# Optimization experiments

Hardware: AMD Instinct MI355X
Metric: run time of the kernel (lower is better)

## Reference

```python
import jax, jax.numpy as jnp
import numpy as np

L1_WEIGHT = 0.5
SSIM_WEIGHT = 0.5
WINDOW_SIZE = 11
SIGMA = 1.5
C1 = 0.01 ** 2
C2 = 0.03 ** 2


def _gaussian_window(dtype):
    coords = jnp.arange(WINDOW_SIZE, dtype=dtype) - (WINDOW_SIZE // 2)
    g = jnp.exp(-(coords ** 2) / (2.0 * SIGMA ** 2))
    g = g / g.sum()
    return g[:, None] * g[None, :]  # (K, K)


def _depthwise_blur(x, win2d):
    # x: (B, C, H, W); depthwise conv with shared Gaussian kernel, SAME padding
    C = x.shape[1]
    kernel = jnp.broadcast_to(win2d[None, None], (C, 1, WINDOW_SIZE, WINDOW_SIZE))
    pad = WINDOW_SIZE // 2
    return jax.lax.conv_general_dilated(
        x, kernel,
        window_strides=(1, 1),
        padding=((pad, pad), (pad, pad)),
        dimension_numbers=("NCHW", "OIHW", "NCHW"),
        feature_group_count=C,
    )


def _ssim(img1, img2):
    win = _gaussian_window(img1.dtype)
    mu1 = _depthwise_blur(img1, win)
    mu2 = _depthwise_blur(img2, win)
    mu1_sq = mu1 * mu1
    mu2_sq = mu2 * mu2
    mu1_mu2 = mu1 * mu2
    sigma1_sq = _depthwise_blur(img1 * img1, win) - mu1_sq
    sigma2_sq = _depthwise_blur(img2 * img2, win) - mu2_sq
    sigma12 = _depthwise_blur(img1 * img2, win) - mu1_mu2
    ssim_map = ((2.0 * mu1_mu2 + C1) * (2.0 * sigma12 + C2)) / (
        (mu1_sq + mu2_sq + C1) * (sigma1_sq + sigma2_sq + C2)
    )
    return ssim_map.mean()


def setup_inputs() -> dict:
    key = jax.random.key(0)
    k1, k2 = jax.random.split(key)
    shape = (32, 3, 512, 512)
    warped = jax.random.uniform(k1, shape, dtype=jnp.float32)
    target = jax.random.uniform(k2, shape, dtype=jnp.float32)
    return {"warped": warped, "target": target}


def reference(warped, target):
    l1_loss = jnp.mean(jnp.abs(warped - target))
    ssim_val = _ssim(warped, target)
    ssim_loss = 1.0 - ssim_val
    total_loss = L1_WEIGHT * l1_loss + SSIM_WEIGHT * ssim_loss
    return total_loss
```

## Files before the change

### kernel.cpp

```cpp
#include <hip/hip_runtime.h>
#include <math.h>

#define IMW 512
#define IMH 512
#define NPIX (IMW * IMH)
#define NBX 8
#define NBY 8
#define NBLK (NBX * NBY * 96)
#define C1F 1.0e-4f
#define C2F 9.0e-4f
#define H2P2 20

typedef short s16x8 __attribute__((ext_vector_type(8)));
typedef float f32x4 __attribute__((ext_vector_type(4)));
typedef float f32x2 __attribute__((ext_vector_type(2)));

__device__ __forceinline__ unsigned cvtpk(float a, float b) {
    unsigned r;
    asm("v_cvt_pk_bf16_f32 %0, %1, %2" : "=v"(r) : "v"(a), "v"(b));
    return r;
}
__device__ __forceinline__ unsigned bf16_rne(float f) {
    unsigned u = __builtin_bit_cast(unsigned, f);
    return (u + 0x7FFFu + ((u >> 16) & 1u)) >> 16;
}
__device__ __forceinline__ float bf16_to_f(unsigned b) {
    return __builtin_bit_cast(float, b << 16);
}
__device__ __forceinline__ f32x4 spl4(float v) { f32x4 r = {v, v, v, v}; return r; }
__device__ __forceinline__ f32x2 spl2(float v) { f32x2 r; r[0] = v; r[1] = v; return r; }
__device__ __forceinline__ f32x2 lo2(f32x4 v) { f32x2 r; r[0] = v[0]; r[1] = v[1]; return r; }
__device__ __forceinline__ f32x2 hi2(f32x4 v) { f32x2 r; r[0] = v[2]; r[1] = v[3]; return r; }

__device__ __forceinline__ f32x2 pk_mul(f32x2 a, f32x2 b) {
    f32x2 d; asm("v_pk_mul_f32 %0, %1, %2" : "=v"(d) : "v"(a), "v"(b)); return d;
}
__device__ __forceinline__ f32x2 pk_add(f32x2 a, f32x2 b) {
    f32x2 d; asm("v_pk_add_f32 %0, %1, %2" : "=v"(d) : "v"(a), "v"(b)); return d;
}
__device__ __forceinline__ f32x2 pk_sub(f32x2 a, f32x2 b) {
    f32x2 d; asm("v_pk_add_f32 %0, %1, %2 neg_lo:[0,1] neg_hi:[0,1]" : "=v"(d) : "v"(a), "v"(b)); return d;
}
__device__ __forceinline__ f32x2 pk_fma(f32x2 a, f32x2 b, f32x2 c) {
    f32x2 d; asm("v_pk_fma_f32 %0, %1, %2, %3" : "=v"(d) : "v"(a), "v"(b), "v"(c)); return d;
}
__device__ __forceinline__ f32x2 abs2(f32x2 a) {
    f32x2 d; d[0] = fabsf(a[0]); d[1] = fabsf(a[1]); return d;
}

__global__ void setup_kernel(uint4* __restrict__ wtab)
{
    const int lane = threadIdx.x;
    const int lane15 = lane & 15;
    const int g = lane >> 4;
    float w[11];
    float s = 0.f;
    for (int i = 0; i < 11; ++i) {
        const float c = (float)(i - 5);
        w[i] = expf(-(c * c) / 4.5f);
        s += w[i];
    }
    for (int i = 0; i < 11; ++i) w[i] /= s;

    s16x8 bwh, bwl, avh, avl;
    #pragma unroll
    for (int e = 0; e < 8; ++e) {
        const int k = 8 * g + e;
        const int th = k - lane15 - 3;
        const float wh = (th >= 0 && th <= 10) ? w[th] : 0.f;
        const int tv = k - lane15;
        const float wvv = (tv >= 0 && tv <= 10) ? w[tv] : 0.f;
        const unsigned h1 = bf16_rne(wh);
        const unsigned l1 = bf16_rne(wh - bf16_to_f(h1));
        bwh[e] = (short)h1; bwl[e] = (short)l1;
        const unsigned h2 = bf16_rne(wvv);
        const unsigned l2 = bf16_rne(wvv - bf16_to_f(h2));
        avh[e] = (short)h2; avl[e] = (short)l2;
    }
    wtab[lane * 4 + 0] = __builtin_bit_cast(uint4, bwh);
    wtab[lane * 4 + 1] = __builtin_bit_cast(uint4, bwl);
    wtab[lane * 4 + 2] = __builtin_bit_cast(uint4, avh);
    wtab[lane * 4 + 3] = __builtin_bit_cast(uint4, avl);
}

__global__ __launch_bounds__(256)
void ssim_l1_kernel(const float* __restrict__ warped,
                    const float* __restrict__ target,
                    const uint4* __restrict__ wtab,
                    float2* __restrict__ partial)
{
    __shared__ unsigned int LDSU[5128];

    const int tid = threadIdx.x;
    const int lane = tid & 63;
    const int wv = tid >> 6;
    const int lane15 = lane & 15;
    const int g = (lane >> 4) & 3;
    const int c0 = blockIdx.x * 64;
    const int r0 = blockIdx.y * 64;
    const size_t base = (size_t)blockIdx.z * NPIX;

    const char* xc = (const char*)(warped + base);
    const char* yc = (const char*)(target + base);

    const s16x8 BwH = __builtin_bit_cast(s16x8, wtab[lane * 4 + 0]);
    const s16x8 BwL = __builtin_bit_cast(s16x8, wtab[lane * 4 + 1]);
    const s16x8 AvH = __builtin_bit_cast(s16x8, wtab[lane * 4 + 2]);
    const s16x8 AvL = __builtin_bit_cast(s16x8, wtab[lane * 4 + 3]);

    const int s0 = 16 * wv + 8 * g;
    const int cb0 = (c0 - 8) * 4;
    const int colb = min(max(cb0 + s0 * 4, 0), 2016);

    f32x4 cw0, cw1, mx0, mx1;
    #pragma unroll
    for (int e = 0; e < 4; ++e) {
        const int sA = s0 + e, sB = sA + 4;
        cw0[e] = (sA < 8 || sA > 71) ? 0.f : ((sA < 16 || sA >= 64) ? 1.f : 0.5f);
        cw1[e] = (sB < 8 || sB > 71) ? 0.f : ((sB < 16 || sB >= 64) ? 1.f : 0.5f);
        const int cA = c0 - 8 + sA, cB = c0 - 8 + sB;
        mx0[e] = ((unsigned)cA < (unsigned)IMW) ? 1.f : 0.f;
        mx1[e] = ((unsigned)cB < (unsigned)IMW) ? 1.f : 0.f;
    }
    const f32x2 cw0lo = lo2(cw0), cw0hi = hi2(cw0);
    const f32x2 cw1lo = lo2(cw1), cw1hi = hi2(cw1);
    const bool edge = (blockIdx.x == 0) || (blockIdx.x == NBX - 1) ||
                      (blockIdx.y == 0) || (blockIdx.y == NBY - 1) ||
                      (colb != cb0 + s0 * 4);

    f32x2 l1a = spl2(0.f), l1b = spl2(0.f);
    f32x2 ssa = spl2(0.f), ssb = spl2(0.f);
    const f32x2 two2 = spl2(2.f), c12 = spl2(C1F), c22 = spl2(C2F);

    const int uoffE = 4 * g;
    const int uoffO = 8 - 8 * (g >> 1) + 4 * (g & 1);

    auto VPASS = [&](int ot) {
        const int uoff = (ot & 1) ? uoffO : uoffE;
        f32x4 V[4];
        __builtin_amdgcn_s_setprio(1);
        #pragma unroll
        for (int q = 0; q < 4; ++q) {
            const uint4 br = *(const uint4*)&LDSU[((wv * 4 + q) * 16 + lane15) * H2P2 + uoff];
            const s16x8 B = __builtin_bit_cast(s16x8, br);
            f32x4 acc = spl4(0.f);
            acc = __builtin_amdgcn_mfma_f32_16x16x32_bf16(AvH, B, acc, 0, 0, 0);
            acc = __builtin_amdgcn_mfma_f32_16x16x32_bf16(AvL, B, acc, 0, 0, 0);
            V[q] = acc;
        }
        __builtin_amdgcn_s_setprio(0);
        #pragma unroll
        for (int h = 0; h < 2; ++h) {
            const f32x2 v0 = h ? hi2(V[0]) : lo2(V[0]);
            const f32x2 v1 = h ? hi2(V[1]) : lo2(V[1]);
            const f32x2 v2 = h ? hi2(V[2]) : lo2(V[2]);
            const f32x2 v3 = h ? hi2(V[3]) : lo2(V[3]);
            const f32x2 mu12  = pk_mul(v0, v1);
            const f32x2 mu1sq = pk_mul(v0, v0);
            const f32x2 mu2sq = pk_mul(v1, v1);
            const f32x2 s12   = pk_sub(v3, mu12);
            const f32x2 ssg   = pk_sub(pk_sub(v2, mu1sq), mu2sq);
            const f32x2 num = pk_mul(pk_fma(two2, mu12, c12), pk_fma(two2, s12, c22));
            const f32x2 den = pk_mul(pk_add(pk_add(mu1sq, mu2sq), c12), pk_add(ssg, c22));
            f32x2 r;
            r[0] = __builtin_amdgcn_rcpf(den[0]);
            r[1] = __builtin_amdgcn_rcpf(den[1]);
            if (h) ssb = pk_fma(num, r, ssb);
            else   ssa = pk_fma(num, r, ssa);
        }
    };

    f32x4 P0[4], P1[4];
    auto LOADB = [&](int t, f32x4* dst) {
        const int rsl = min(max(r0 - 5 + 16 * t + lane15, 0), IMH - 1);
        const char* px = xc + (size_t)rsl * (IMW * 4) + colb;
        const char* py = yc + (size_t)rsl * (IMW * 4) + colb;
        dst[0] = *(const f32x4*)px;
        dst[1] = *(const f32x4*)(px + 16);
        dst[2] = *(const f32x4*)py;
        dst[3] = *(const f32x4*)(py + 16);
    };

    LOADB(0, P0);
    LOADB(1, P1);

    #pragma unroll
    for (int t = 0; t < 5; ++t) {
        f32x4* B = (t & 1) ? P1 : P0;
        f32x4 x0 = B[0], x1 = B[1], y0 = B[2], y1 = B[3];
        if (t + 2 < 5) LOADB(t + 2, B);

        if (edge) {
            const float rr = ((unsigned)(r0 - 5 + 16 * t + lane15) < (unsigned)IMH) ? 1.f : 0.f;
            const f32x4 m0 = mx0 * spl4(rr);
            const f32x4 m1 = mx1 * spl4(rr);
            x0 *= m0; x1 *= m1; y0 *= m0; y1 *= m1;
        }

        {
            const float rmL1 = (t == 0) ? ((lane15 >= 5) ? 1.f : 0.f)
                             : (t == 4) ? ((lane15 <= 4) ? 1.f : 0.f)
                             : 1.f;
            const f32x2 rm2 = spl2(rmL1);
            const f32x2 t0 = abs2(pk_sub(lo2(x0), lo2(y0)));
            const f32x2 t1 = abs2(pk_sub(hi2(x0), hi2(y0)));
            const f32x2 t2 = abs2(pk_sub(lo2(x1), lo2(y1)));
            const f32x2 t3 = abs2(pk_sub(hi2(x1), hi2(y1)));
            const f32x2 s01 = pk_fma(cw0lo, t0, pk_mul(cw1lo, t2));
            const f32x2 s23 = pk_fma(cw0hi, t1, pk_mul(cw1hi, t3));
            l1a = pk_fma(s01, rm2, l1a);
            l1b = pk_fma(s23, rm2, l1b);
        }

        const f32x2 q2al = pk_fma(lo2(x0), lo2(x0), pk_mul(lo2(y0), lo2(y0)));
        const f32x2 q2ah = pk_fma(hi2(x0), hi2(x0), pk_mul(hi2(y0), hi2(y0)));
        const f32x2 q2bl = pk_fma(lo2(x1), lo2(x1), pk_mul(lo2(y1), lo2(y1)));
        const f32x2 q2bh = pk_fma(hi2(x1), hi2(x1), pk_mul(hi2(y1), hi2(y1)));
        const f32x2 q3al = pk_mul(lo2(x0), lo2(y0));
        const f32x2 q3ah = pk_mul(hi2(x0), hi2(y0));
        const f32x2 q3bl = pk_mul(lo2(x1), lo2(y1));
        const f32x2 q3bh = pk_mul(hi2(x1), hi2(y1));

        uint4 A0u, A1u, A2u, A3u;
        A0u.x = cvtpk(x0[0], x0[1]); A0u.y = cvtpk(x0[2], x0[3]);
        A0u.z = cvtpk(x1[0], x1[1]); A0u.w = cvtpk(x1[2], x1[3]);
        A1u.x = cvtpk(y0[0], y0[1]); A1u.y = cvtpk(y0[2], y0[3]);
        A1u.z = cvtpk(y1[0], y1[1]); A1u.w = cvtpk(y1[2], y1[3]);
        A2u.x = cvtpk(q2al[0], q2al[1]); A2u.y = cvtpk(q2ah[0], q2ah[1]);
        A2u.z = cvtpk(q2bl[0], q2bl[1]); A2u.w = cvtpk(q2bh[0], q2bh[1]);
        A3u.x = cvtpk(q3al[0], q3al[1]); A3u.y = cvtpk(q3ah[0], q3ah[1]);
        A3u.z = cvtpk(q3bl[0], q3bl[1]); A3u.w = cvtpk(q3bh[0], q3bh[1]);

        const s16x8 A0 = __builtin_bit_cast(s16x8, A0u);
        const s16x8 A1 = __builtin_bit_cast(s16x8, A1u);
        const s16x8 A2 = __builtin_bit_cast(s16x8, A2u);
        const s16x8 A3 = __builtin_bit_cast(s16x8, A3u);

        f32x4 C0 = spl4(0.f), C1 = spl4(0.f), C2 = spl4(0.f), C3 = spl4(0.f);
        __builtin_amdgcn_s_setprio(1);
        C0 = __builtin_amdgcn_mfma_f32_16x16x32_bf16(A0, BwH, C0, 0, 0, 0);
        C0 = __builtin_amdgcn_mfma_f32_16x16x32_bf16(A0, BwL, C0, 0, 0, 0);
        C1 = __builtin_amdgcn_mfma_f32_16x16x32_bf16(A1, BwH, C1, 0, 0, 0);
        C1 = __builtin_amdgcn_mfma_f32_16x16x32_bf16(A1, BwL, C1, 0, 0, 0);
        C2 = __builtin_amdgcn_mfma_f32_16x16x32_bf16(A2, BwH, C2, 0, 0, 0);
        C2 = __builtin_amdgcn_mfma_f32_16x16x32_bf16(A2, BwL, C2, 0, 0, 0);
        C3 = __builtin_amdgcn_mfma_f32_16x16x32_bf16(A3, BwH, C3, 0, 0, 0);
        C3 = __builtin_amdgcn_mfma_f32_16x16x32_bf16(A3, BwL, C3, 0, 0, 0);
        __builtin_amdgcn_s_setprio(0);

        #pragma unroll
        for (int q = 0; q < 4; ++q) {
            const f32x4 Cq = (q == 0) ? C0 : (q == 1) ? C1 : (q == 2) ? C2 : C3;
            uint2 pp;
            pp.x = cvtpk(Cq[0], Cq[1]);
            pp.y = cvtpk(Cq[2], Cq[3]);
            *(uint2*)&LDSU[((wv * 4 + q) * 16 + lane15) * H2P2 + (t & 1) * 8 + 2 * g] = pp;
        }

        if (t >= 1) VPASS(t - 1);
    }

    float l1sum = (l1a[0] + l1a[1]) + (l1b[0] + l1b[1]);
    float ssum  = (ssa[0] + ssa[1]) + (ssb[0] + ssb[1]);
    #pragma unroll
    for (int off = 32; off > 0; off >>= 1) {
        l1sum += __shfl_down(l1sum, off);
        ssum  += __shfl_down(ssum,  off);
    }
    float* red = (float*)&LDSU[5120];
    if (lane == 0) { red[wv] = l1sum; red[4 + wv] = ssum; }
    __syncthreads();
    if (tid == 0) {
        const float L1 = red[0] + red[1] + red[2] + red[3];
        const float SS = red[4] + red[5] + red[6] + red[7];
        const int bid = (blockIdx.z * gridDim.y + blockIdx.y) * gridDim.x + blockIdx.x;
        partial[bid] = make_float2(L1, SS);
    }
}

__global__ __launch_bounds__(256)
void reduce_kernel(const float2* __restrict__ partial, float* __restrict__ out)
{
    double l1 = 0.0, ss = 0.0;
    for (int i = threadIdx.x; i < NBLK; i += 256) {
        const float2 p = partial[i];
        l1 += (double)p.x;
        ss += (double)p.y;
    }
    #pragma unroll
    for (int off = 32; off > 0; off >>= 1) {
        l1 += __shfl_down(l1, off);
        ss += __shfl_down(ss, off);
    }
    __shared__ double red[8];
    const int wv = threadIdx.x >> 6, lane = threadIdx.x & 63;
    if (lane == 0) { red[wv] = l1; red[4 + wv] = ss; }
    __syncthreads();
    if (threadIdx.x == 0) {
        const double n = 25165824.0;
        const double L1 = (red[0] + red[1] + red[2] + red[3]) / n;
        const double SS = (red[4] + red[5] + red[6] + red[7]) / n;
        out[0] = (float)(0.5 * L1 + 0.5 * (1.0 - SS));
    }
}

extern "C" void kernel_launch(void* const* d_in, const int* in_sizes, int n_in,
                              void* d_out, int out_size, void* d_ws, size_t ws_size,
                              hipStream_t stream)
{
    const float* warped = (const float*)d_in[0];
    const float* target = (const float*)d_in[1];
    float* out = (float*)d_out;
    uint4* wtab = (uint4*)d_ws;
    float2* partial = (float2*)((char*)d_ws + 4096);

    hipLaunchKernelGGL(setup_kernel, dim3(1), dim3(64), 0, stream, wtab);
    hipLaunchKernelGGL(ssim_l1_kernel, dim3(NBX, NBY, 96), dim3(256), 0, stream,
                       warped, target, wtab, partial);
    hipLaunchKernelGGL(reduce_kernel, dim3(1), dim3(256), 0, stream, partial, out);
}
```

Measured before the change: 80.58 us.

## Stage input tiles through LDS via global_load_lds with XOR-swizzled layout

Replaces the per-thread register double-buffered global loads with direct global-to-LDS async loads (global_load_lds, 16 bytes per lane). Each wave gets its own double-buffered region, and reads use an XOR swizzle so that rows land in coalesced 16-byte chunks without bank conflicts. The aim is cheaper load issue, fewer registers spent on prefetch buffers, and better coalescing. The cost is a much larger LDS footprint, which may lower occupancy, plus manual vmcnt/lgkmcnt waits that add scheduling constraints.

```diff
diff --git a/kernel.cpp b/kernel.cpp
--- a/kernel.cpp
+++ b/kernel.cpp
@@ -9,6 +9,7 @@
 #define NBLK (NBX * NBY * 96)
 #define C1F 1.0e-4f
 #define C2F 9.0e-4f
+#define H2B 8192
 #define H2P2 20
 
 typedef short s16x8 __attribute__((ext_vector_type(8)));
@@ -26,6 +27,12 @@
 }
 __device__ __forceinline__ float bf16_to_f(unsigned b) {
     return __builtin_bit_cast(float, b << 16);
+}
+__device__ __forceinline__ void gload16(const void* g, void* l) {
+    __builtin_amdgcn_global_load_lds(
+        (const __attribute__((address_space(1))) void*)g,
+        (__attribute__((address_space(3))) void*)l,
+        16, 0, 0);
 }
 __device__ __forceinline__ f32x4 spl4(float v) { f32x4 r = {v, v, v, v}; return r; }
 __device__ __forceinline__ f32x2 spl2(float v) { f32x2 r; r[0] = v; r[1] = v; return r; }
@@ -89,7 +96,7 @@
                     const uint4* __restrict__ wtab,
                     float2* __restrict__ partial)
 {
-    __shared__ unsigned int LDSU[5128];
+    __shared__ unsigned int LDSU[13320];
 
     const int tid = threadIdx.x;
     const int lane = tid & 63;
@@ -99,6 +106,8 @@
     const int c0 = blockIdx.x * 64;
     const int r0 = blockIdx.y * 64;
     const size_t base = (size_t)blockIdx.z * NPIX;
+    char* LB = (char*)LDSU;
+    char* SB = LB + wv * 8192;
 
     const char* xc = (const char*)(warped + base);
     const char* yc = (const char*)(target + base);
@@ -108,25 +117,45 @@
     const s16x8 AvH = __builtin_bit_cast(s16x8, wtab[lane * 4 + 2]);
     const s16x8 AvL = __builtin_bit_cast(s16x8, wtab[lane * 4 + 3]);
 
+    const int wcb0 = (c0 - 8 + 16 * wv) * 4;
+    const int row0 = lane >> 3;
+    const int row1 = row0 + 8;
+    const int gl   = lane & 7;
+    const int scol0 = min(max(wcb0 + ((gl ^ (row0 & 7)) << 4), 0), 2032);
+    const int scol1 = min(max(wcb0 + ((gl ^ (row1 & 7)) << 4), 0), 2032);
+    const int lo0 = lane * 16;
+    const int lo1 = lane * 16 + 1024;
+
+    auto STAGE = [&](int t, int b) {
+        const int rbase = r0 - 5 + 16 * t;
+        const size_t rb0 = (size_t)min(max(rbase + row0, 0), IMH - 1) * 2048;
+        const size_t rb1 = (size_t)min(max(rbase + row1, 0), IMH - 1) * 2048;
+        char* db = SB + b * 4096;
+        gload16(xc + rb0 + scol0, db + lo0);
+        gload16(xc + rb1 + scol1, db + lo1);
+        gload16(yc + rb0 + scol0, db + 2048 + lo0);
+        gload16(yc + rb1 + scol1, db + 2048 + lo1);
+    };
+
+    const unsigned roff = (unsigned)(lane15 * 128);
+    const unsigned gA = (unsigned)((((2 * g)    ) ^ (lane15 & 7)) * 16);
+    const unsigned gB = (unsigned)((((2 * g) + 1) ^ (lane15 & 7)) * 16);
+
     const int s0 = 16 * wv + 8 * g;
-    const int cb0 = (c0 - 8) * 4;
-    const int colb = min(max(cb0 + s0 * 4, 0), 2016);
-
     f32x4 cw0, cw1, mx0, mx1;
     #pragma unroll
     for (int e = 0; e < 4; ++e) {
-        const int sA = s0 + e, sB = sA + 4;
+        const int sA = s0 + e, sB2 = sA + 4;
         cw0[e] = (sA < 8 || sA > 71) ? 0.f : ((sA < 16 || sA >= 64) ? 1.f : 0.5f);
-        cw1[e] = (sB < 8 || sB > 71) ? 0.f : ((sB < 16 || sB >= 64) ? 1.f : 0.5f);
-        const int cA = c0 - 8 + sA, cB = c0 - 8 + sB;
+        cw1[e] = (sB2 < 8 || sB2 > 71) ? 0.f : ((sB2 < 16 || sB2 >= 64) ? 1.f : 0.5f);
+        const int cA = c0 - 8 + sA, cB = c0 - 8 + sB2;
         mx0[e] = ((unsigned)cA < (unsigned)IMW) ? 1.f : 0.f;
         mx1[e] = ((unsigned)cB < (unsigned)IMW) ? 1.f : 0.f;
     }
     const f32x2 cw0lo = lo2(cw0), cw0hi = hi2(cw0);
     const f32x2 cw1lo = lo2(cw1), cw1hi = hi2(cw1);
     const bool edge = (blockIdx.x == 0) || (blockIdx.x == NBX - 1) ||
-                      (blockIdx.y == 0) || (blockIdx.y == NBY - 1) ||
-                      (colb != cb0 + s0 * 4);
+                      (blockIdx.y == 0) || (blockIdx.y == NBY - 1);
 
     f32x2 l1a = spl2(0.f), l1b = spl2(0.f);
     f32x2 ssa = spl2(0.f), ssb = spl2(0.f);
@@ -141,7 +170,7 @@
         __builtin_amdgcn_s_setprio(1);
         #pragma unroll
         for (int q = 0; q < 4; ++q) {
-            const uint4 br = *(const uint4*)&LDSU[((wv * 4 + q) * 16 + lane15) * H2P2 + uoff];
+            const uint4 br = *(const uint4*)&LDSU[H2B + ((wv * 4 + q) * 16 + lane15) * H2P2 + uoff];
             const s16x8 B = __builtin_bit_cast(s16x8, br);
             f32x4 acc = spl4(0.f);
             acc = __builtin_amdgcn_mfma_f32_16x16x32_bf16(AvH, B, acc, 0, 0, 0);
@@ -170,25 +199,27 @@
         }
     };
 
-    f32x4 P0[4], P1[4];
-    auto LOADB = [&](int t, f32x4* dst) {
-        const int rsl = min(max(r0 - 5 + 16 * t + lane15, 0), IMH - 1);
-        const char* px = xc + (size_t)rsl * (IMW * 4) + colb;
-        const char* py = yc + (size_t)rsl * (IMW * 4) + colb;
-        dst[0] = *(const f32x4*)px;
-        dst[1] = *(const f32x4*)(px + 16);
-        dst[2] = *(const f32x4*)py;
-        dst[3] = *(const f32x4*)(py + 16);
-    };
-
-    LOADB(0, P0);
-    LOADB(1, P1);
+    STAGE(0, 0);
+    STAGE(1, 1);
+    __builtin_amdgcn_sched_barrier(0);
 
     #pragma unroll
     for (int t = 0; t < 5; ++t) {
-        f32x4* B = (t & 1) ? P1 : P0;
-        f32x4 x0 = B[0], x1 = B[1], y0 = B[2], y1 = B[3];
-        if (t + 2 < 5) LOADB(t + 2, B);
+        if (t < 4) asm volatile("s_waitcnt vmcnt(4)" ::: "memory");
+        else       asm volatile("s_waitcnt vmcnt(0)" ::: "memory");
+
+        const char* pb = SB + (t & 1) * 4096;
+        f32x4 x0 = *(const f32x4*)(pb + roff + gA);
+        f32x4 x1 = *(const f32x4*)(pb + roff + gB);
+        f32x4 y0 = *(const f32x4*)(pb + 2048 + roff + gA);
+        f32x4 y1 = *(const f32x4*)(pb + 2048 + roff + gB);
+
+        asm volatile("s_waitcnt lgkmcnt(0)" ::: "memory");
+        __builtin_amdgcn_sched_barrier(0);
+        if (t + 2 <= 4) {
+            STAGE(t + 2, t & 1);
+            __builtin_amdgcn_sched_barrier(0);
+        }
 
         if (edge) {
             const float rr = ((unsigned)(r0 - 5 + 16 * t + lane15) < (unsigned)IMH) ? 1.f : 0.f;
@@ -254,7 +285,7 @@
             uint2 pp;
             pp.x = cvtpk(Cq[0], Cq[1]);
             pp.y = cvtpk(Cq[2], Cq[3]);
-            *(uint2*)&LDSU[((wv * 4 + q) * 16 + lane15) * H2P2 + (t & 1) * 8 + 2 * g] = pp;
+            *(uint2*)&LDSU[H2B + ((wv * 4 + q) * 16 + lane15) * H2P2 + (t & 1) * 8 + 2 * g] = pp;
         }
 
         if (t >= 1) VPASS(t - 1);
@@ -267,7 +298,7 @@
         l1sum += __shfl_down(l1sum, off);
         ssum  += __shfl_down(ssum,  off);
     }
-    float* red = (float*)&LDSU[5120];
+    float* red = (float*)&LDSU[13312];
     if (lane == 0) { red[wv] = l1sum; red[4 + wv] = ssum; }
     __syncthreads();
     if (tid == 0) {
```

After: 78.07 us. -3.1%, faster.
